# Kernel optimization log

Hardware: AMD Instinct MI355X
Metric: run time of the kernel (lower is better)

Reference implementation:

```python
import jax, jax.numpy as jnp
import numpy as np

D_MODEL = 1024
NUM_HEADS = 16
HEAD_DIM = D_MODEL // NUM_HEADS


def setup_inputs() -> dict:
    key = jax.random.key(0)
    ks = jax.random.split(key, 9)
    B, T = 2, 2048
    s = 1.0 / np.sqrt(D_MODEL)
    return {
        "x": jax.random.normal(ks[0], (B, T, D_MODEL), dtype=jnp.float32),
        "Wq": jax.random.normal(ks[1], (D_MODEL, D_MODEL), dtype=jnp.float32) * s,
        "bq": jnp.zeros((D_MODEL,), dtype=jnp.float32),
        "Wk": jax.random.normal(ks[2], (D_MODEL, D_MODEL), dtype=jnp.float32) * s,
        "bk": jnp.zeros((D_MODEL,), dtype=jnp.float32),
        "Wv": jax.random.normal(ks[3], (D_MODEL, D_MODEL), dtype=jnp.float32) * s,
        "bv": jnp.zeros((D_MODEL,), dtype=jnp.float32),
        "Wo": jax.random.normal(ks[4], (D_MODEL, D_MODEL), dtype=jnp.float32) * s,
        "bo": jnp.zeros((D_MODEL,), dtype=jnp.float32),
    }


def reference(x, Wq, bq, Wk, bk, Wv, bv, Wo, bo):
    B, T, D = x.shape
    H, Hd = NUM_HEADS, HEAD_DIM
    # Linear projections; weights stored as [in, out] (torch Linear transposed)
    q = (x @ Wq + bq).reshape(B, T, H, Hd)
    k = (x @ Wk + bk).reshape(B, T, H, Hd)
    v = (x @ Wv + bv).reshape(B, T, H, Hd)
    scale = 1.0 / jnp.sqrt(jnp.asarray(Hd, dtype=x.dtype))
    scores = jnp.einsum("bqhd,bkhd->bhqk", q, k) * scale  # [B,H,T,T]
    attn = jax.nn.softmax(scores, axis=-1)
    ctx = jnp.einsum("bhqk,bkhd->bqhd", attn, v).reshape(B, T, D)
    return ctx @ Wo + bo
```

## Files before the change

kernel.cpp:

```cpp
#include <hip/hip_runtime.h>


typedef unsigned short ushort_t;
typedef __attribute__((ext_vector_type(8))) short bf16x8;
typedef __attribute__((ext_vector_type(4))) short bf16x4;
typedef __attribute__((ext_vector_type(4))) float f32x4;

#define BATCH 2
#define SEQ   2048
#define DM    1024
#define NH    16
#define HD    64
#define MTOT  (BATCH*SEQ)

#if __has_builtin(__builtin_amdgcn_exp2f)
#define EXP2(x) __builtin_amdgcn_exp2f(x)
#else
#define EXP2(x) exp2f(x)
#endif

__device__ __forceinline__ ushort_t f2bf(float f) {
    union { float f; unsigned int u; } v; v.f = f;
    unsigned int r = v.u + 0x7fffu + ((v.u >> 16) & 1u);
    return (ushort_t)(r >> 16);
}

__device__ __forceinline__ void gload_lds16(const void* g, void* l) {
    __builtin_amdgcn_global_load_lds(
        (const __attribute__((address_space(1))) unsigned int*)g,
        (__attribute__((address_space(3))) unsigned int*)l, 16, 0, 0);
}

__global__ __launch_bounds__(256) void prep_kernel(const float* __restrict__ x,
                                                   const float* __restrict__ W0,
                                                   const float* __restrict__ W1,
                                                   const float* __restrict__ W2,
                                                   const float* __restrict__ W3,
                                                   ushort_t* __restrict__ xb,
                                                   ushort_t* __restrict__ Wtb) {
    __shared__ ushort_t tile[64][72];
    int bid = blockIdx.x, tid = threadIdx.x;
    if (bid < 4096) {
        int i = bid * 256 + tid;
        float4 v = ((const float4*)x)[i];
        ushort4 o;
        o.x = f2bf(v.x); o.y = f2bf(v.y); o.z = f2bf(v.z); o.w = f2bf(v.w);
        ((ushort4*)xb)[i] = o;
        return;
    }
    int b2 = bid - 4096;
    const float* Ws[4] = {W0, W1, W2, W3};
    const float* W = Ws[b2 >> 8];
    ushort_t* Wt = Wtb + (size_t)(b2 >> 8) * DM * DM;
    int k0 = ((b2 >> 4) & 15) * 64, n0 = (b2 & 15) * 64;
    int tr = tid >> 4;
    int tc = (tid & 15) * 4;
#pragma unroll
    for (int j = 0; j < 4; j++) {
        int r = j * 16 + tr;
        float4 v = *(const float4*)&W[(size_t)(k0 + r) * DM + n0 + tc];
        tile[r][tc + 0] = f2bf(v.x); tile[r][tc + 1] = f2bf(v.y);
        tile[r][tc + 2] = f2bf(v.z); tile[r][tc + 3] = f2bf(v.w);
    }
    __syncthreads();
#pragma unroll
    for (int j = 0; j < 4; j++) {
        int n = j * 16 + tr;
        ushort4 o;
        o.x = tile[tc + 0][n]; o.y = tile[tc + 1][n];
        o.z = tile[tc + 2][n]; o.w = tile[tc + 3][n];
        *(ushort4*)&Wt[(size_t)(n0 + n) * DM + k0 + tc] = o;
    }
}

__global__ __launch_bounds__(256) void gemm_qkv(const ushort_t* __restrict__ A,
                                                const ushort_t* __restrict__ Wtb,
                                                const float* __restrict__ bq,
                                                const float* __restrict__ bk,
                                                const float* __restrict__ bv,
                                                ushort_t* __restrict__ qo,
                                                ushort_t* __restrict__ ko,
                                                ushort_t* __restrict__ vo) {
    __shared__ ushort_t As[3][128 * 32];
    __shared__ ushort_t Bs[3][128 * 32];
    int sel = blockIdx.x >> 3;
    const ushort_t* Wt = Wtb + (size_t)sel * DM * DM;
    const float* bias = sel == 0 ? bq : (sel == 1 ? bk : bv);
    int tid = threadIdx.x;
    int w = tid >> 6, lane = tid & 63, lr = lane & 15, lg = lane >> 4;
    int wr = w >> 1, wc = w & 1;
    int m0 = blockIdx.y * 128, n0 = (blockIdx.x & 7) * 128;

    int srow = (w * 2) * 16 + (lane >> 2);
    int scb = (lane & 3) * 8;
    const ushort_t* ag = &A[(size_t)(m0 + srow) * DM + scb];
    const ushort_t* bg = &Wt[(size_t)(n0 + srow) * DM + scb];
    int ldst = (w * 2) * 1024;

    f32x4 acc[4][4] = {};

#pragma unroll
    for (int p = 0; p < 2; p++) {
        gload_lds16(ag + (size_t)p * 16 * DM, (char*)As[0] + ldst + p * 1024);
        gload_lds16(bg + (size_t)p * 16 * DM, (char*)Bs[0] + ldst + p * 1024);
    }

    int cur = 0;
    for (int kt = 0; kt < 32; ++kt) {
        if (kt + 1 < 32) {
            int nxt = cur + 1 == 3 ? 0 : cur + 1;
            int k0 = (kt + 1) << 5;
#pragma unroll
            for (int p = 0; p < 2; p++) {
                gload_lds16(ag + (size_t)p * 16 * DM + k0, (char*)As[nxt] + ldst + p * 1024);
                gload_lds16(bg + (size_t)p * 16 * DM + k0, (char*)Bs[nxt] + ldst + p * 1024);
            }
            __builtin_amdgcn_sched_barrier(0);
            asm volatile("s_waitcnt vmcnt(4)" ::: "memory");
        } else {
            __builtin_amdgcn_sched_barrier(0);
            asm volatile("s_waitcnt vmcnt(0)" ::: "memory");
        }
        __builtin_amdgcn_s_barrier();
        __builtin_amdgcn_sched_barrier(0);

        bf16x8 af[4], bfr[4];
#pragma unroll
        for (int i = 0; i < 4; i++) {
            af[i]  = *(const bf16x8*)&As[cur][(wr * 64 + i * 16 + lr) * 32 + lg * 8];
            bfr[i] = *(const bf16x8*)&Bs[cur][(wc * 64 + i * 16 + lr) * 32 + lg * 8];
        }
#pragma unroll
        for (int mi = 0; mi < 4; mi++)
#pragma unroll
            for (int ni = 0; ni < 4; ni++)
                acc[mi][ni] = __builtin_amdgcn_mfma_f32_16x16x32_bf16(
                    af[mi], bfr[ni], acc[mi][ni], 0, 0, 0);
        cur = cur + 1 == 3 ? 0 : cur + 1;
    }

    float scale = (sel == 0) ? 0.125f * 1.44269504f : 1.0f;
#pragma unroll
    for (int mi = 0; mi < 4; mi++) {
#pragma unroll
        for (int ni = 0; ni < 4; ni++) {
            f32x4 a = acc[mi][ni];
            int n = n0 + wc * 64 + ni * 16 + lr;
            float bs = bias[n];
            int mbase = m0 + wr * 64 + mi * 16 + lg * 4;
            int hh = n >> 6, d = n & 63;
            if (sel == 2) {
                int b = mbase >> 11, tt = mbase & 2047;
                size_t base = ((size_t)(b * NH + hh) * HD + d) * SEQ + tt;
                ushort4 pk;
                pk.x = f2bf(a[0] + bs); pk.y = f2bf(a[1] + bs);
                pk.z = f2bf(a[2] + bs); pk.w = f2bf(a[3] + bs);
                *(ushort4*)&vo[base] = pk;
            } else {
                ushort_t* o = sel ? ko : qo;
#pragma unroll
                for (int r = 0; r < 4; r++) {
                    int m = mbase + r;
                    int b = m >> 11, tt = m & 2047;
                    o[((size_t)(b * NH + hh) * SEQ + tt) * HD + d] =
                        f2bf((a[r] + bs) * scale);
                }
            }
        }
    }
}

__global__ __launch_bounds__(256) void gemm_out(const ushort_t* __restrict__ A,
                                                const ushort_t* __restrict__ Wt,
                                                const float* __restrict__ bias,
                                                float* __restrict__ out) {
    __shared__ ushort_t As[3][128 * 32];
    __shared__ ushort_t Bs[3][128 * 32];
    int tid = threadIdx.x;
    int w = tid >> 6, lane = tid & 63, lr = lane & 15, lg = lane >> 4;
    int wr = w >> 1, wc = w & 1;
    int m0 = blockIdx.y * 128, n0 = blockIdx.x * 128;

    int srow = (w * 2) * 16 + (lane >> 2);
    int scb = (lane & 3) * 8;
    const ushort_t* ag = &A[(size_t)(m0 + srow) * DM + scb];
    const ushort_t* bg = &Wt[(size_t)(n0 + srow) * DM + scb];
    int ldst = (w * 2) * 1024;

    f32x4 acc[4][4] = {};

#pragma unroll
    for (int p = 0; p < 2; p++) {
        gload_lds16(ag + (size_t)p * 16 * DM, (char*)As[0] + ldst + p * 1024);
        gload_lds16(bg + (size_t)p * 16 * DM, (char*)Bs[0] + ldst + p * 1024);
    }

    int cur = 0;
    for (int kt = 0; kt < 32; ++kt) {
        if (kt + 1 < 32) {
            int nxt = cur + 1 == 3 ? 0 : cur + 1;
            int k0 = (kt + 1) << 5;
#pragma unroll
            for (int p = 0; p < 2; p++) {
                gload_lds16(ag + (size_t)p * 16 * DM + k0, (char*)As[nxt] + ldst + p * 1024);
                gload_lds16(bg + (size_t)p * 16 * DM + k0, (char*)Bs[nxt] + ldst + p * 1024);
            }
            __builtin_amdgcn_sched_barrier(0);
            asm volatile("s_waitcnt vmcnt(4)" ::: "memory");
        } else {
            __builtin_amdgcn_sched_barrier(0);
            asm volatile("s_waitcnt vmcnt(0)" ::: "memory");
        }
        __builtin_amdgcn_s_barrier();
        __builtin_amdgcn_sched_barrier(0);

        bf16x8 af[4], bfr[4];
#pragma unroll
        for (int i = 0; i < 4; i++) {
            af[i]  = *(const bf16x8*)&As[cur][(wr * 64 + i * 16 + lr) * 32 + lg * 8];
            bfr[i] = *(const bf16x8*)&Bs[cur][(wc * 64 + i * 16 + lr) * 32 + lg * 8];
        }
#pragma unroll
        for (int mi = 0; mi < 4; mi++)
#pragma unroll
            for (int ni = 0; ni < 4; ni++)
                acc[mi][ni] = __builtin_amdgcn_mfma_f32_16x16x32_bf16(
                    af[mi], bfr[ni], acc[mi][ni], 0, 0, 0);
        cur = cur + 1 == 3 ? 0 : cur + 1;
    }

#pragma unroll
    for (int mi = 0; mi < 4; mi++) {
#pragma unroll
        for (int ni = 0; ni < 4; ni++) {
            f32x4 a = acc[mi][ni];
            int n = n0 + wc * 64 + ni * 16 + lr;
            float bs = bias[n];
            int mbase = m0 + wr * 64 + mi * 16 + lg * 4;
#pragma unroll
            for (int r = 0; r < 4; r++)
                out[(size_t)(mbase + r) * DM + n] = a[r] + bs;
        }
    }
}

__device__ __forceinline__ void softmax_pack(f32x4 (&s)[8], float& l_run,
                                             int4 (&pwv)[4]) {
    float rs0 = 0.f, rs1 = 0.f, rs2 = 0.f, rs3 = 0.f;
#pragma unroll
    for (int nt = 0; nt < 8; ++nt) {
        float p0 = EXP2(s[nt][0]);
        float p1 = EXP2(s[nt][1]);
        float p2 = EXP2(s[nt][2]);
        float p3 = EXP2(s[nt][3]);
        s[nt][0] = p0; s[nt][1] = p1; s[nt][2] = p2; s[nt][3] = p3;
        rs0 += p0; rs1 += p1; rs2 += p2; rs3 += p3;
    }
    float rs = (rs0 + rs1) + (rs2 + rs3);
    rs += __shfl_xor(rs, 16);
    rs += __shfl_xor(rs, 32);
    l_run += rs;
#pragma unroll
    for (int kk = 0; kk < 4; ++kk) {
        unsigned pw[4];
#pragma unroll
        for (int hh = 0; hh < 2; ++hh)
#pragma unroll
            for (int pr = 0; pr < 2; ++pr) {
                unsigned rr;
                asm("v_cvt_pk_bf16_f32 %0, %1, %2"
                    : "=v"(rr)
                    : "v"(s[kk + 4 * hh][2 * pr]), "v"(s[kk + 4 * hh][2 * pr + 1]));
                pw[hh * 2 + pr] = rr;
            }
        pwv[kk] = make_int4(pw[0], pw[1], pw[2], pw[3]);
    }
}

__global__ __launch_bounds__(512, 2) void attn_kernel(const ushort_t* __restrict__ Q,
                                                      const ushort_t* __restrict__ Kb,
                                                      const ushort_t* __restrict__ Vt,
                                                      ushort_t* __restrict__ Ctx) {
    __shared__ ushort_t Ks[2][128 * 64];
    __shared__ ushort_t Vs[2][64 * 128];

    int tid = threadIdx.x, w = tid >> 6, lane = tid & 63, lr = lane & 15, lg = lane >> 4;
    int orig = blockIdx.x;
    int wg = (orig & 7) * 32 + (orig >> 3);
    int qb = wg & 7, bh = wg >> 3;
    int q0 = qb * 256;

    const ushort_t* Qp = Q + (size_t)bh * SEQ * HD;
    const ushort_t* Kp = Kb + (size_t)bh * SEQ * HD;
    const ushort_t* Vp = Vt + (size_t)bh * HD * SEQ;

    int qrow = q0 + w * 16 + lr;
    bf16x8 aqA[2], aqB[2];
    aqA[0] = *(const bf16x8*)&Qp[(size_t)qrow * HD + lg * 8];
    aqA[1] = *(const bf16x8*)&Qp[(size_t)qrow * HD + 32 + lg * 8];
    aqB[0] = *(const bf16x8*)&Qp[(size_t)(qrow + 128) * HD + lg * 8];
    aqB[1] = *(const bf16x8*)&Qp[(size_t)(qrow + 128) * HD + 32 + lg * 8];

    f32x4 oaccA[4] = {}, oaccB[4] = {};
    float lA = 0.f, lB = 0.f;

    int krow = tid >> 3, kch = tid & 7;
    int kbyte = krow * 128 + ((kch * 16) ^ ((krow & 7) << 4));
    const ushort_t* kg0 = &Kp[(size_t)krow * HD + kch * 8];
    const ushort_t* kg1 = &Kp[(size_t)(krow + 64) * HD + kch * 8];
    int vrow = tid >> 4, vch = tid & 15;
    int S_a2 = (((vch >> 1) & 3) * 32 + (vch & 1) * 16 + (vch >> 3) * 4) * 2;
    int vswz = (vrow & 7) << 4;
    int vbyte0 = vrow * 256 + (S_a2 ^ vswz);
    int vbyte1 = vrow * 256 + ((S_a2 + 16) ^ vswz);
    const ushort_t* vg0 = &Vp[(size_t)vrow * SEQ + vch * 8];
    const ushort_t* vg1 = &Vp[(size_t)(vrow + 32) * SEQ + vch * 8];

    {
        bf16x8 k0v = *(const bf16x8*)kg0;
        bf16x8 k1v = *(const bf16x8*)kg1;
        bf16x8 v0v = *(const bf16x8*)vg0;
        bf16x8 v1v = *(const bf16x8*)vg1;
        *(bf16x8*)((char*)Ks[0] + kbyte) = k0v;
        *(bf16x8*)((char*)Ks[0] + kbyte + 64 * 128) = k1v;
        union { bf16x8 v; bf16x4 h[2]; } u0, u1;
        u0.v = v0v; u1.v = v1v;
        *(bf16x4*)((char*)Vs[0] + vbyte0) = u0.h[0];
        *(bf16x4*)((char*)Vs[0] + vbyte1) = u0.h[1];
        *(bf16x4*)((char*)Vs[0] + vbyte0 + 32 * 256) = u1.h[0];
        *(bf16x4*)((char*)Vs[0] + vbyte1 + 32 * 256) = u1.h[1];
    }
    __syncthreads();

    int kread = lr * 128;
    int kswz = (lr & 7) << 4;

    for (int t = 0; t < SEQ / 128; ++t) {
        int cur = t & 1;
        bf16x8 kr0, kr1, vr0, vr1;
        bool more = (t + 1 < SEQ / 128);
        if (more) {
            size_t ko_off = (size_t)(t + 1) * 128 * HD;
            int vo_off = (t + 1) * 128;
            kr0 = *(const bf16x8*)(kg0 + ko_off);
            kr1 = *(const bf16x8*)(kg1 + ko_off);
            vr0 = *(const bf16x8*)(vg0 + vo_off);
            vr1 = *(const bf16x8*)(vg1 + vo_off);
        }

        f32x4 sA[8], sB[8];
        __builtin_amdgcn_s_setprio(1);
#pragma unroll
        for (int nt = 0; nt < 8; ++nt) {
            f32x4 a = {}, b = {};
#pragma unroll
            for (int kk = 0; kk < 2; ++kk) {
                bf16x8 bk = *(const bf16x8*)((char*)Ks[cur] + nt * 2048 + kread +
                                             ((kk * 64 + lg * 16) ^ kswz));
                a = __builtin_amdgcn_mfma_f32_16x16x32_bf16(bk, aqA[kk], a, 0, 0, 0);
                b = __builtin_amdgcn_mfma_f32_16x16x32_bf16(bk, aqB[kk], b, 0, 0, 0);
            }
            sA[nt] = a; sB[nt] = b;
        }
        __builtin_amdgcn_s_setprio(0);

        int4 pwvA[4], pwvB[4];
        softmax_pack(sA, lA, pwvA);
        softmax_pack(sB, lB, pwvB);

        __builtin_amdgcn_s_setprio(1);
#pragma unroll
        for (int dt = 0; dt < 4; ++dt) {
            int vbase = (dt * 16 + lr) * 256;
#pragma unroll
            for (int kk = 0; kk < 4; ++kk) {
                bf16x8 bv = *(const bf16x8*)((char*)Vs[cur] + vbase +
                                             ((kk * 64 + lg * 16) ^ kswz));
                oaccA[dt] = __builtin_amdgcn_mfma_f32_16x16x32_bf16(
                    *(bf16x8*)&pwvA[kk], bv, oaccA[dt], 0, 0, 0);
                oaccB[dt] = __builtin_amdgcn_mfma_f32_16x16x32_bf16(
                    *(bf16x8*)&pwvB[kk], bv, oaccB[dt], 0, 0, 0);
            }
        }
        __builtin_amdgcn_s_setprio(0);

        if (more) {
            char* kd = (char*)Ks[cur ^ 1];
            char* vd = (char*)Vs[cur ^ 1];
            *(bf16x8*)(kd + kbyte) = kr0;
            *(bf16x8*)(kd + kbyte + 64 * 128) = kr1;
            union { bf16x8 v; bf16x4 h[2]; } u0, u1;
            u0.v = vr0; u1.v = vr1;
            *(bf16x4*)(vd + vbyte0) = u0.h[0];
            *(bf16x4*)(vd + vbyte1) = u0.h[1];
            *(bf16x4*)(vd + vbyte0 + 32 * 256) = u1.h[0];
            *(bf16x4*)(vd + vbyte1 + 32 * 256) = u1.h[1];
            __syncthreads();
        }
    }

    float invA = 1.0f / lA, invB = 1.0f / lB;
    float ivA[4], ivB[4];
#pragma unroll
    for (int r = 0; r < 4; ++r) {
        ivA[r] = __shfl(invA, lg * 4 + r);
        ivB[r] = __shfl(invB, lg * 4 + r);
    }
    int b = bh >> 4, h = bh & 15;
#pragma unroll
    for (int dt = 0; dt < 4; ++dt)
#pragma unroll
        for (int r = 0; r < 4; ++r) {
            int q = q0 + w * 16 + lg * 4 + r;
            Ctx[((size_t)(b * SEQ + q)) * DM + h * HD + dt * 16 + lr] =
                f2bf(oaccA[dt][r] * ivA[r]);
            Ctx[((size_t)(b * SEQ + q + 128)) * DM + h * HD + dt * 16 + lr] =
                f2bf(oaccB[dt][r] * ivB[r]);
        }
}

extern "C" void kernel_launch(void* const* d_in, const int* in_sizes, int n_in,
                              void* d_out, int out_size, void* d_ws, size_t ws_size,
                              hipStream_t stream) {
    const float* x  = (const float*)d_in[0];
    const float* Wq = (const float*)d_in[1];
    const float* bq = (const float*)d_in[2];
    const float* Wk = (const float*)d_in[3];
    const float* bk = (const float*)d_in[4];
    const float* Wv = (const float*)d_in[5];
    const float* bv = (const float*)d_in[6];
    const float* Wo = (const float*)d_in[7];
    const float* bo = (const float*)d_in[8];
    float* out = (float*)d_out;

    ushort_t* xbf = (ushort_t*)d_ws;
    ushort_t* wtb = xbf + (size_t)MTOT * DM;
    ushort_t* qbf = wtb + (size_t)4 * DM * DM;
    ushort_t* kbf = qbf + (size_t)MTOT * DM;
    ushort_t* vtb = kbf + (size_t)MTOT * DM;
    ushort_t* ctx = vtb + (size_t)MTOT * DM;

    prep_kernel<<<4096 + 1024, 256, 0, stream>>>(x, Wq, Wk, Wv, Wo, xbf, wtb);

    gemm_qkv<<<dim3(24, 32), 256, 0, stream>>>(xbf, wtb, bq, bk, bv, qbf, kbf, vtb);

    attn_kernel<<<256, 512, 0, stream>>>(qbf, kbf, vtb, ctx);

    gemm_out<<<dim3(8, 32), 256, 0, stream>>>(ctx, wtb + (size_t)3 * DM * DM, bo, out);
}
```

Before: 119.0 us.

## Software-pipeline attention: overlap previous tile's PV MFMAs with current QK

Restructures the attention KV loop so each iteration first computes QK^T scores for tile t, then runs the P·V MFMAs for tile t-1, and only then does softmax for tile t. The goal is to keep the matrix units busy while the exp/max softmax work runs, rather than serialising QK, softmax and PV. V gets a third LDS buffer because the previous tile's V must stay live while the next one is written. The loop is unrolled by two to ping-pong the packed P registers, with a final PV step after the loop. In exchange it uses more LDS and more registers per block, which risks spills under the 512-thread, 2-blocks-per-CU launch bound.

```diff
diff --git a/kernel.cpp b/kernel.cpp
--- a/kernel.cpp
+++ b/kernel.cpp
@@ -12,6 +12,7 @@
 #define NH    16
 #define HD    64
 #define MTOT  (BATCH*SEQ)
+#define NTILE (SEQ/128)
 
 #if __has_builtin(__builtin_amdgcn_exp2f)
 #define EXP2(x) __builtin_amdgcn_exp2f(x)
@@ -277,12 +278,88 @@
     }
 }
 
+__device__ __forceinline__ void attn_tile(
+    int t, bool first,
+    const ushort_t* kg0, const ushort_t* kg1,
+    const ushort_t* vg0, const ushort_t* vg1,
+    char* KsB, char* VsB,
+    int kbyte, int vbyte0, int vbyte1, int kread, int kswz, int lg,
+    bf16x8 (&aqA)[2], bf16x8 (&aqB)[2],
+    f32x4 (&oaccA)[4], f32x4 (&oaccB)[4], float& lA, float& lB,
+    int4 (&ppA)[4], int4 (&ppB)[4],
+    int4 (&opA)[4], int4 (&opB)[4])
+{
+    bool more = (t + 1 < NTILE);
+    bf16x8 kr0, kr1, vr0, vr1;
+    if (more) {
+        size_t ko_off = (size_t)(t + 1) * 128 * HD;
+        int vo_off = (t + 1) * 128;
+        kr0 = *(const bf16x8*)(kg0 + ko_off);
+        kr1 = *(const bf16x8*)(kg1 + ko_off);
+        vr0 = *(const bf16x8*)(vg0 + vo_off);
+        vr1 = *(const bf16x8*)(vg1 + vo_off);
+    }
+
+    char* KsCur = KsB + (t & 1) * 16384;
+    f32x4 sA[8], sB[8];
+    __builtin_amdgcn_s_setprio(1);
+#pragma unroll
+    for (int nt = 0; nt < 8; ++nt) {
+        f32x4 a = {}, b = {};
+#pragma unroll
+        for (int kk = 0; kk < 2; ++kk) {
+            bf16x8 bk = *(const bf16x8*)(KsCur + nt * 2048 + kread +
+                                         ((kk * 64 + lg * 16) ^ kswz));
+            a = __builtin_amdgcn_mfma_f32_16x16x32_bf16(bk, aqA[kk], a, 0, 0, 0);
+            b = __builtin_amdgcn_mfma_f32_16x16x32_bf16(bk, aqB[kk], b, 0, 0, 0);
+        }
+        sA[nt] = a; sB[nt] = b;
+    }
+    __builtin_amdgcn_s_setprio(0);
+
+    if (!first) {
+        char* VsPrev = VsB + ((t + 2) % 3) * 16384;
+        __builtin_amdgcn_s_setprio(1);
+#pragma unroll
+        for (int dt = 0; dt < 4; ++dt) {
+            int vbase = (dt * 16 + (kread >> 7)) * 256;
+#pragma unroll
+            for (int kk = 0; kk < 4; ++kk) {
+                bf16x8 bv = *(const bf16x8*)(VsPrev + vbase +
+                                             ((kk * 64 + lg * 16) ^ kswz));
+                oaccA[dt] = __builtin_amdgcn_mfma_f32_16x16x32_bf16(
+                    *(bf16x8*)&ppA[kk], bv, oaccA[dt], 0, 0, 0);
+                oaccB[dt] = __builtin_amdgcn_mfma_f32_16x16x32_bf16(
+                    *(bf16x8*)&ppB[kk], bv, oaccB[dt], 0, 0, 0);
+            }
+        }
+        __builtin_amdgcn_s_setprio(0);
+    }
+
+    softmax_pack(sA, lA, opA);
+    softmax_pack(sB, lB, opB);
+
+    if (more) {
+        char* kd = KsB + ((t + 1) & 1) * 16384;
+        char* vd = VsB + ((t + 1) % 3) * 16384;
+        *(bf16x8*)(kd + kbyte) = kr0;
+        *(bf16x8*)(kd + kbyte + 64 * 128) = kr1;
+        union { bf16x8 v; bf16x4 h[2]; } u0, u1;
+        u0.v = vr0; u1.v = vr1;
+        *(bf16x4*)(vd + vbyte0) = u0.h[0];
+        *(bf16x4*)(vd + vbyte1) = u0.h[1];
+        *(bf16x4*)(vd + vbyte0 + 32 * 256) = u1.h[0];
+        *(bf16x4*)(vd + vbyte1 + 32 * 256) = u1.h[1];
+        __syncthreads();
+    }
+}
+
 __global__ __launch_bounds__(512, 2) void attn_kernel(const ushort_t* __restrict__ Q,
                                                       const ushort_t* __restrict__ Kb,
                                                       const ushort_t* __restrict__ Vt,
                                                       ushort_t* __restrict__ Ctx) {
     __shared__ ushort_t Ks[2][128 * 64];
-    __shared__ ushort_t Vs[2][64 * 128];
+    __shared__ ushort_t Vs[3][64 * 128];
 
     int tid = threadIdx.x, w = tid >> 6, lane = tid & 63, lr = lane & 15, lg = lane >> 4;
     int orig = blockIdx.x;
@@ -334,68 +411,40 @@
 
     int kread = lr * 128;
     int kswz = (lr & 7) << 4;
-
-    for (int t = 0; t < SEQ / 128; ++t) {
-        int cur = t & 1;
-        bf16x8 kr0, kr1, vr0, vr1;
-        bool more = (t + 1 < SEQ / 128);
-        if (more) {
-            size_t ko_off = (size_t)(t + 1) * 128 * HD;
-            int vo_off = (t + 1) * 128;
-            kr0 = *(const bf16x8*)(kg0 + ko_off);
-            kr1 = *(const bf16x8*)(kg1 + ko_off);
-            vr0 = *(const bf16x8*)(vg0 + vo_off);
-            vr1 = *(const bf16x8*)(vg1 + vo_off);
-        }
-
-        f32x4 sA[8], sB[8];
-        __builtin_amdgcn_s_setprio(1);
-#pragma unroll
-        for (int nt = 0; nt < 8; ++nt) {
-            f32x4 a = {}, b = {};
-#pragma unroll
-            for (int kk = 0; kk < 2; ++kk) {
-                bf16x8 bk = *(const bf16x8*)((char*)Ks[cur] + nt * 2048 + kread +
-                                             ((kk * 64 + lg * 16) ^ kswz));
-                a = __builtin_amdgcn_mfma_f32_16x16x32_bf16(bk, aqA[kk], a, 0, 0, 0);
-                b = __builtin_amdgcn_mfma_f32_16x16x32_bf16(bk, aqB[kk], b, 0, 0, 0);
-            }
-            sA[nt] = a; sB[nt] = b;
-        }
-        __builtin_amdgcn_s_setprio(0);
-
-        int4 pwvA[4], pwvB[4];
-        softmax_pack(sA, lA, pwvA);
-        softmax_pack(sB, lB, pwvB);
-
-        __builtin_amdgcn_s_setprio(1);
+    char* KsB = (char*)Ks[0];
+    char* VsB = (char*)Vs[0];
+
+    int4 pA0[4], pB0[4], pA1[4], pB1[4];
+
+    attn_tile(0, true, kg0, kg1, vg0, vg1, KsB, VsB, kbyte, vbyte0, vbyte1,
+              kread, kswz, lg, aqA, aqB, oaccA, oaccB, lA, lB,
+              pA1, pB1, pA0, pB0);
+    for (int t = 1; t < NTILE - 1; t += 2) {
+        attn_tile(t, false, kg0, kg1, vg0, vg1, KsB, VsB, kbyte, vbyte0, vbyte1,
+                  kread, kswz, lg, aqA, aqB, oaccA, oaccB, lA, lB,
+                  pA0, pB0, pA1, pB1);
+        attn_tile(t + 1, false, kg0, kg1, vg0, vg1, KsB, VsB, kbyte, vbyte0, vbyte1,
+                  kread, kswz, lg, aqA, aqB, oaccA, oaccB, lA, lB,
+                  pA1, pB1, pA0, pB0);
+    }
+    attn_tile(NTILE - 1, false, kg0, kg1, vg0, vg1, KsB, VsB, kbyte, vbyte0, vbyte1,
+              kread, kswz, lg, aqA, aqB, oaccA, oaccB, lA, lB,
+              pA0, pB0, pA1, pB1);
+
+    {
+        char* VsLast = VsB + ((NTILE - 1) % 3) * 16384;
 #pragma unroll
         for (int dt = 0; dt < 4; ++dt) {
             int vbase = (dt * 16 + lr) * 256;
 #pragma unroll
             for (int kk = 0; kk < 4; ++kk) {
-                bf16x8 bv = *(const bf16x8*)((char*)Vs[cur] + vbase +
+                bf16x8 bv = *(const bf16x8*)(VsLast + vbase +
                                              ((kk * 64 + lg * 16) ^ kswz));
                 oaccA[dt] = __builtin_amdgcn_mfma_f32_16x16x32_bf16(
-                    *(bf16x8*)&pwvA[kk], bv, oaccA[dt], 0, 0, 0);
+                    *(bf16x8*)&pA1[kk], bv, oaccA[dt], 0, 0, 0);
                 oaccB[dt] = __builtin_amdgcn_mfma_f32_16x16x32_bf16(
-                    *(bf16x8*)&pwvB[kk], bv, oaccB[dt], 0, 0, 0);
-            }
-        }
-        __builtin_amdgcn_s_setprio(0);
-
-        if (more) {
-            char* kd = (char*)Ks[cur ^ 1];
-            char* vd = (char*)Vs[cur ^ 1];
-            *(bf16x8*)(kd + kbyte) = kr0;
-            *(bf16x8*)(kd + kbyte + 64 * 128) = kr1;
-            union { bf16x8 v; bf16x4 h[2]; } u0, u1;
-            u0.v = vr0; u1.v = vr1;
-            *(bf16x4*)(vd + vbyte0) = u0.h[0];
-            *(bf16x4*)(vd + vbyte1) = u0.h[1];
-            *(bf16x4*)(vd + vbyte0 + 32 * 256) = u1.h[0];
-            *(bf16x4*)(vd + vbyte1 + 32 * 256) = u1.h[1];
-            __syncthreads();
+                    *(bf16x8*)&pB1[kk], bv, oaccB[dt], 0, 0, 0);
+            }
         }
     }
 
```

Result: no change. 119.4 us (+0.3%).

## Switch attention kernel to 32x32x16 MFMA tiles with reworked V LDS layout

Applied to the files above, without the earlier changes.

Rewrites the attention inner loop to use 32x32x16 bf16 MFMA instructions instead of pairs of 16x16x32. Each wave now owns 32 contiguous query rows, and the K/V LDS read patterns and the V write swizzle are changed to match the new operand layout. The softmax row-sum needs only one cross-lane shuffle instead of two. The larger MFMA tile reduces instruction count and LDS operand reads per FLOP, but it changes register usage and risks layout bugs in the new index math.

```diff
diff --git a/kernel.cpp b/kernel.cpp
--- a/kernel.cpp
+++ b/kernel.cpp
@@ -5,6 +5,7 @@
 typedef __attribute__((ext_vector_type(8))) short bf16x8;
 typedef __attribute__((ext_vector_type(4))) short bf16x4;
 typedef __attribute__((ext_vector_type(4))) float f32x4;
+typedef __attribute__((ext_vector_type(16))) float f32x16;
 
 #define BATCH 2
 #define SEQ   2048
@@ -12,6 +13,7 @@
 #define NH    16
 #define HD    64
 #define MTOT  (BATCH*SEQ)
+#define NTILE (SEQ/128)
 
 #if __has_builtin(__builtin_amdgcn_exp2f)
 #define EXP2(x) __builtin_amdgcn_exp2f(x)
@@ -244,39 +246,6 @@
     }
 }
 
-__device__ __forceinline__ void softmax_pack(f32x4 (&s)[8], float& l_run,
-                                             int4 (&pwv)[4]) {
-    float rs0 = 0.f, rs1 = 0.f, rs2 = 0.f, rs3 = 0.f;
-#pragma unroll
-    for (int nt = 0; nt < 8; ++nt) {
-        float p0 = EXP2(s[nt][0]);
-        float p1 = EXP2(s[nt][1]);
-        float p2 = EXP2(s[nt][2]);
-        float p3 = EXP2(s[nt][3]);
-        s[nt][0] = p0; s[nt][1] = p1; s[nt][2] = p2; s[nt][3] = p3;
-        rs0 += p0; rs1 += p1; rs2 += p2; rs3 += p3;
-    }
-    float rs = (rs0 + rs1) + (rs2 + rs3);
-    rs += __shfl_xor(rs, 16);
-    rs += __shfl_xor(rs, 32);
-    l_run += rs;
-#pragma unroll
-    for (int kk = 0; kk < 4; ++kk) {
-        unsigned pw[4];
-#pragma unroll
-        for (int hh = 0; hh < 2; ++hh)
-#pragma unroll
-            for (int pr = 0; pr < 2; ++pr) {
-                unsigned rr;
-                asm("v_cvt_pk_bf16_f32 %0, %1, %2"
-                    : "=v"(rr)
-                    : "v"(s[kk + 4 * hh][2 * pr]), "v"(s[kk + 4 * hh][2 * pr + 1]));
-                pw[hh * 2 + pr] = rr;
-            }
-        pwv[kk] = make_int4(pw[0], pw[1], pw[2], pw[3]);
-    }
-}
-
 __global__ __launch_bounds__(512, 2) void attn_kernel(const ushort_t* __restrict__ Q,
                                                       const ushort_t* __restrict__ Kb,
                                                       const ushort_t* __restrict__ Vt,
@@ -284,7 +253,9 @@
     __shared__ ushort_t Ks[2][128 * 64];
     __shared__ ushort_t Vs[2][64 * 128];
 
-    int tid = threadIdx.x, w = tid >> 6, lane = tid & 63, lr = lane & 15, lg = lane >> 4;
+    int tid = threadIdx.x, w = tid >> 6, lane = tid & 63;
+    int lq = lane & 31;
+    int kh = lane >> 5;
     int orig = blockIdx.x;
     int wg = (orig & 7) * 32 + (orig >> 3);
     int qb = wg & 7, bh = wg >> 3;
@@ -294,25 +265,24 @@
     const ushort_t* Kp = Kb + (size_t)bh * SEQ * HD;
     const ushort_t* Vp = Vt + (size_t)bh * HD * SEQ;
 
-    int qrow = q0 + w * 16 + lr;
-    bf16x8 aqA[2], aqB[2];
-    aqA[0] = *(const bf16x8*)&Qp[(size_t)qrow * HD + lg * 8];
-    aqA[1] = *(const bf16x8*)&Qp[(size_t)qrow * HD + 32 + lg * 8];
-    aqB[0] = *(const bf16x8*)&Qp[(size_t)(qrow + 128) * HD + lg * 8];
-    aqB[1] = *(const bf16x8*)&Qp[(size_t)(qrow + 128) * HD + 32 + lg * 8];
-
-    f32x4 oaccA[4] = {}, oaccB[4] = {};
-    float lA = 0.f, lB = 0.f;
+    int qrow = q0 + w * 32 + lq;
+    bf16x8 aq[4];
+#pragma unroll
+    for (int c = 0; c < 4; ++c)
+        aq[c] = *(const bf16x8*)&Qp[(size_t)qrow * HD + c * 16 + kh * 8];
+
+    f32x16 oacc0 = {}, oacc1 = {};
+    float l_run = 0.f;
 
     int krow = tid >> 3, kch = tid & 7;
     int kbyte = krow * 128 + ((kch * 16) ^ ((krow & 7) << 4));
     const ushort_t* kg0 = &Kp[(size_t)krow * HD + kch * 8];
     const ushort_t* kg1 = &Kp[(size_t)(krow + 64) * HD + kch * 8];
     int vrow = tid >> 4, vch = tid & 15;
-    int S_a2 = (((vch >> 1) & 3) * 32 + (vch & 1) * 16 + (vch >> 3) * 4) * 2;
+    int B0 = 64 * (vch >> 2) + 32 * ((vch >> 1) & 1) + 8 * (vch & 1);
     int vswz = (vrow & 7) << 4;
-    int vbyte0 = vrow * 256 + (S_a2 ^ vswz);
-    int vbyte1 = vrow * 256 + ((S_a2 + 16) ^ vswz);
+    int vbyte0 = vrow * 256 + (B0 ^ vswz);
+    int vbyte1 = vrow * 256 + ((B0 + 16) ^ vswz);
     const ushort_t* vg0 = &Vp[(size_t)vrow * SEQ + vch * 8];
     const ushort_t* vg1 = &Vp[(size_t)(vrow + 32) * SEQ + vch * 8];
 
@@ -332,13 +302,12 @@
     }
     __syncthreads();
 
-    int kread = lr * 128;
-    int kswz = (lr & 7) << 4;
-
-    for (int t = 0; t < SEQ / 128; ++t) {
+    int lsw = (lq & 7) << 4;
+
+    for (int t = 0; t < NTILE; ++t) {
         int cur = t & 1;
         bf16x8 kr0, kr1, vr0, vr1;
-        bool more = (t + 1 < SEQ / 128);
+        bool more = (t + 1 < NTILE);
         if (more) {
             size_t ko_off = (size_t)(t + 1) * 128 * HD;
             int vo_off = (t + 1) * 128;
@@ -348,39 +317,62 @@
             vr1 = *(const bf16x8*)(vg1 + vo_off);
         }
 
-        f32x4 sA[8], sB[8];
+        f32x16 s[4];
         __builtin_amdgcn_s_setprio(1);
 #pragma unroll
-        for (int nt = 0; nt < 8; ++nt) {
-            f32x4 a = {}, b = {};
-#pragma unroll
-            for (int kk = 0; kk < 2; ++kk) {
-                bf16x8 bk = *(const bf16x8*)((char*)Ks[cur] + nt * 2048 + kread +
-                                             ((kk * 64 + lg * 16) ^ kswz));
-                a = __builtin_amdgcn_mfma_f32_16x16x32_bf16(bk, aqA[kk], a, 0, 0, 0);
-                b = __builtin_amdgcn_mfma_f32_16x16x32_bf16(bk, aqB[kk], b, 0, 0, 0);
-            }
-            sA[nt] = a; sB[nt] = b;
+        for (int tau = 0; tau < 4; ++tau) {
+            f32x16 a = {};
+            int kb = (tau * 32 + lq) * 128;
+#pragma unroll
+            for (int c = 0; c < 4; ++c) {
+                bf16x8 ak = *(const bf16x8*)((char*)Ks[cur] + kb +
+                                             ((c * 32 + kh * 16) ^ lsw));
+                a = __builtin_amdgcn_mfma_f32_32x32x16_bf16(ak, aq[c], a, 0, 0, 0);
+            }
+            s[tau] = a;
         }
         __builtin_amdgcn_s_setprio(0);
 
-        int4 pwvA[4], pwvB[4];
-        softmax_pack(sA, lA, pwvA);
-        softmax_pack(sB, lB, pwvB);
+        int4 pp[8];
+        float rsum = 0.f;
+#pragma unroll
+        for (int tau = 0; tau < 4; ++tau) {
+            float pe[16];
+            float r0 = 0.f, r1 = 0.f, r2 = 0.f, r3 = 0.f;
+#pragma unroll
+            for (int e = 0; e < 16; e += 4) {
+                pe[e + 0] = EXP2(s[tau][e + 0]);
+                pe[e + 1] = EXP2(s[tau][e + 1]);
+                pe[e + 2] = EXP2(s[tau][e + 2]);
+                pe[e + 3] = EXP2(s[tau][e + 3]);
+                r0 += pe[e + 0]; r1 += pe[e + 1];
+                r2 += pe[e + 2]; r3 += pe[e + 3];
+            }
+            rsum += (r0 + r1) + (r2 + r3);
+            unsigned pw0[4], pw1[4];
+#pragma unroll
+            for (int wd = 0; wd < 4; ++wd) {
+                asm("v_cvt_pk_bf16_f32 %0, %1, %2"
+                    : "=v"(pw0[wd]) : "v"(pe[2 * wd]), "v"(pe[2 * wd + 1]));
+                asm("v_cvt_pk_bf16_f32 %0, %1, %2"
+                    : "=v"(pw1[wd]) : "v"(pe[8 + 2 * wd]), "v"(pe[8 + 2 * wd + 1]));
+            }
+            pp[2 * tau]     = make_int4(pw0[0], pw0[1], pw0[2], pw0[3]);
+            pp[2 * tau + 1] = make_int4(pw1[0], pw1[1], pw1[2], pw1[3]);
+        }
+        rsum += __shfl_xor(rsum, 32);
+        l_run += rsum;
 
         __builtin_amdgcn_s_setprio(1);
 #pragma unroll
-        for (int dt = 0; dt < 4; ++dt) {
-            int vbase = (dt * 16 + lr) * 256;
-#pragma unroll
-            for (int kk = 0; kk < 4; ++kk) {
-                bf16x8 bv = *(const bf16x8*)((char*)Vs[cur] + vbase +
-                                             ((kk * 64 + lg * 16) ^ kswz));
-                oaccA[dt] = __builtin_amdgcn_mfma_f32_16x16x32_bf16(
-                    *(bf16x8*)&pwvA[kk], bv, oaccA[dt], 0, 0, 0);
-                oaccB[dt] = __builtin_amdgcn_mfma_f32_16x16x32_bf16(
-                    *(bf16x8*)&pwvB[kk], bv, oaccB[dt], 0, 0, 0);
-            }
+        for (int c = 0; c < 8; ++c) {
+            int vb0 = lq * 256 + ((c * 32 + kh * 16) ^ lsw);
+            bf16x8 bv0 = *(const bf16x8*)((char*)Vs[cur] + vb0);
+            bf16x8 bv1 = *(const bf16x8*)((char*)Vs[cur] + vb0 + 32 * 256);
+            oacc0 = __builtin_amdgcn_mfma_f32_32x32x16_bf16(
+                *(bf16x8*)&pp[c], bv0, oacc0, 0, 0, 0);
+            oacc1 = __builtin_amdgcn_mfma_f32_32x32x16_bf16(
+                *(bf16x8*)&pp[c], bv1, oacc1, 0, 0, 0);
         }
         __builtin_amdgcn_s_setprio(0);
 
@@ -399,24 +391,17 @@
         }
     }
 
-    float invA = 1.0f / lA, invB = 1.0f / lB;
-    float ivA[4], ivB[4];
-#pragma unroll
-    for (int r = 0; r < 4; ++r) {
-        ivA[r] = __shfl(invA, lg * 4 + r);
-        ivB[r] = __shfl(invB, lg * 4 + r);
-    }
-    int b = bh >> 4, h = bh & 15;
-#pragma unroll
-    for (int dt = 0; dt < 4; ++dt)
-#pragma unroll
-        for (int r = 0; r < 4; ++r) {
-            int q = q0 + w * 16 + lg * 4 + r;
-            Ctx[((size_t)(b * SEQ + q)) * DM + h * HD + dt * 16 + lr] =
-                f2bf(oaccA[dt][r] * ivA[r]);
-            Ctx[((size_t)(b * SEQ + q + 128)) * DM + h * HD + dt * 16 + lr] =
-                f2bf(oaccB[dt][r] * ivB[r]);
-        }
+    float inv = 1.0f / l_run;
+    int b = bh >> 4, hd_ = bh & 15;
+#pragma unroll
+    for (int r = 0; r < 16; ++r) {
+        int qloc = (r & 3) + 8 * (r >> 2) + 4 * kh;
+        float iv = __shfl(inv, qloc);
+        int q = q0 + w * 32 + qloc;
+        size_t base = ((size_t)(b * SEQ + q)) * DM + hd_ * HD + lq;
+        Ctx[base]      = f2bf(oacc0[r] * iv);
+        Ctx[base + 32] = f2bf(oacc1[r] * iv);
+    }
 }
 
 extern "C" void kernel_launch(void* const* d_in, const int* in_sizes, int n_in,
```

Result: no change. 121.2 us (+1.8%).

## Drop LDS staging in attention; read K and pre-tiled V directly from global

Applied to the files above, without the earlier changes.

The QKV projection now writes V in a per-128-key tiled layout with the permutation the PV MFMA operand expects, so the attention kernel can load V fragments straight from global memory. The attention kernel drops the shared-memory double buffer and barriers and reads K and V fragments directly from global (L2/cache) inside the loop. It also splits the QK/softmax into separate A and B passes to cut live registers. This removes LDS writes and syncs but relies on cache for the reuse that LDS gave across the eight waves, which risks more global traffic and exposed load latency.

```diff
diff --git a/kernel.cpp b/kernel.cpp
--- a/kernel.cpp
+++ b/kernel.cpp
@@ -3,7 +3,6 @@
 
 typedef unsigned short ushort_t;
 typedef __attribute__((ext_vector_type(8))) short bf16x8;
-typedef __attribute__((ext_vector_type(4))) short bf16x4;
 typedef __attribute__((ext_vector_type(4))) float f32x4;
 
 #define BATCH 2
@@ -12,6 +11,7 @@
 #define NH    16
 #define HD    64
 #define MTOT  (BATCH*SEQ)
+#define NTILE (SEQ/128)
 
 #if __has_builtin(__builtin_amdgcn_exp2f)
 #define EXP2(x) __builtin_amdgcn_exp2f(x)
@@ -151,7 +151,11 @@
             int hh = n >> 6, d = n & 63;
             if (sel == 2) {
                 int b = mbase >> 11, tt = mbase & 2047;
-                size_t base = ((size_t)(b * NH + hh) * HD + d) * SEQ + tt;
+                int kap = tt & 127;
+                int slot = 32 * ((kap >> 4) & 3) + 8 * ((kap >> 2) & 3) + 4 * (kap >> 6);
+                size_t base = (size_t)(b * NH + hh) * SEQ * HD
+                            + (size_t)(tt >> 7) * (128 * HD)
+                            + (size_t)d * 128 + slot;
                 ushort4 pk;
                 pk.x = f2bf(a[0] + bs); pk.y = f2bf(a[1] + bs);
                 pk.z = f2bf(a[2] + bs); pk.w = f2bf(a[3] + bs);
@@ -281,9 +285,6 @@
                                                       const ushort_t* __restrict__ Kb,
                                                       const ushort_t* __restrict__ Vt,
                                                       ushort_t* __restrict__ Ctx) {
-    __shared__ ushort_t Ks[2][128 * 64];
-    __shared__ ushort_t Vs[2][64 * 128];
-
     int tid = threadIdx.x, w = tid >> 6, lane = tid & 63, lr = lane & 15, lg = lane >> 4;
     int orig = blockIdx.x;
     int wg = (orig & 7) * 32 + (orig >> 3);
@@ -292,7 +293,7 @@
 
     const ushort_t* Qp = Q + (size_t)bh * SEQ * HD;
     const ushort_t* Kp = Kb + (size_t)bh * SEQ * HD;
-    const ushort_t* Vp = Vt + (size_t)bh * HD * SEQ;
+    const ushort_t* Vp = Vt + (size_t)bh * SEQ * HD;
 
     int qrow = q0 + w * 16 + lr;
     bf16x8 aqA[2], aqB[2];
@@ -304,99 +305,58 @@
     f32x4 oaccA[4] = {}, oaccB[4] = {};
     float lA = 0.f, lB = 0.f;
 
-    int krow = tid >> 3, kch = tid & 7;
-    int kbyte = krow * 128 + ((kch * 16) ^ ((krow & 7) << 4));
-    const ushort_t* kg0 = &Kp[(size_t)krow * HD + kch * 8];
-    const ushort_t* kg1 = &Kp[(size_t)(krow + 64) * HD + kch * 8];
-    int vrow = tid >> 4, vch = tid & 15;
-    int S_a2 = (((vch >> 1) & 3) * 32 + (vch & 1) * 16 + (vch >> 3) * 4) * 2;
-    int vswz = (vrow & 7) << 4;
-    int vbyte0 = vrow * 256 + (S_a2 ^ vswz);
-    int vbyte1 = vrow * 256 + ((S_a2 + 16) ^ vswz);
-    const ushort_t* vg0 = &Vp[(size_t)vrow * SEQ + vch * 8];
-    const ushort_t* vg1 = &Vp[(size_t)(vrow + 32) * SEQ + vch * 8];
-
-    {
-        bf16x8 k0v = *(const bf16x8*)kg0;
-        bf16x8 k1v = *(const bf16x8*)kg1;
-        bf16x8 v0v = *(const bf16x8*)vg0;
-        bf16x8 v1v = *(const bf16x8*)vg1;
-        *(bf16x8*)((char*)Ks[0] + kbyte) = k0v;
-        *(bf16x8*)((char*)Ks[0] + kbyte + 64 * 128) = k1v;
-        union { bf16x8 v; bf16x4 h[2]; } u0, u1;
-        u0.v = v0v; u1.v = v1v;
-        *(bf16x4*)((char*)Vs[0] + vbyte0) = u0.h[0];
-        *(bf16x4*)((char*)Vs[0] + vbyte1) = u0.h[1];
-        *(bf16x4*)((char*)Vs[0] + vbyte0 + 32 * 256) = u1.h[0];
-        *(bf16x4*)((char*)Vs[0] + vbyte1 + 32 * 256) = u1.h[1];
-    }
-    __syncthreads();
-
-    int kread = lr * 128;
-    int kswz = (lr & 7) << 4;
-
-    for (int t = 0; t < SEQ / 128; ++t) {
-        int cur = t & 1;
-        bf16x8 kr0, kr1, vr0, vr1;
-        bool more = (t + 1 < SEQ / 128);
-        if (more) {
-            size_t ko_off = (size_t)(t + 1) * 128 * HD;
-            int vo_off = (t + 1) * 128;
-            kr0 = *(const bf16x8*)(kg0 + ko_off);
-            kr1 = *(const bf16x8*)(kg1 + ko_off);
-            vr0 = *(const bf16x8*)(vg0 + vo_off);
-            vr1 = *(const bf16x8*)(vg1 + vo_off);
-        }
-
-        f32x4 sA[8], sB[8];
+    for (int t = 0; t < NTILE; ++t) {
+        const ushort_t* Kt = Kp + (size_t)t * 128 * HD;
+        const ushort_t* Vtl = Vp + (size_t)t * 128 * HD;
+
+        f32x4 sA[8];
         __builtin_amdgcn_s_setprio(1);
 #pragma unroll
         for (int nt = 0; nt < 8; ++nt) {
-            f32x4 a = {}, b = {};
+            f32x4 a = {};
 #pragma unroll
             for (int kk = 0; kk < 2; ++kk) {
-                bf16x8 bk = *(const bf16x8*)((char*)Ks[cur] + nt * 2048 + kread +
-                                             ((kk * 64 + lg * 16) ^ kswz));
+                bf16x8 bk = *(const bf16x8*)&Kt[(size_t)(nt * 16 + lr) * HD +
+                                                kk * 32 + lg * 8];
                 a = __builtin_amdgcn_mfma_f32_16x16x32_bf16(bk, aqA[kk], a, 0, 0, 0);
+            }
+            sA[nt] = a;
+        }
+        __builtin_amdgcn_s_setprio(0);
+        int4 ppA[4];
+        softmax_pack(sA, lA, ppA);
+
+        f32x4 sB[8];
+        __builtin_amdgcn_s_setprio(1);
+#pragma unroll
+        for (int nt = 0; nt < 8; ++nt) {
+            f32x4 b = {};
+#pragma unroll
+            for (int kk = 0; kk < 2; ++kk) {
+                bf16x8 bk = *(const bf16x8*)&Kt[(size_t)(nt * 16 + lr) * HD +
+                                                kk * 32 + lg * 8];
                 b = __builtin_amdgcn_mfma_f32_16x16x32_bf16(bk, aqB[kk], b, 0, 0, 0);
             }
-            sA[nt] = a; sB[nt] = b;
+            sB[nt] = b;
         }
         __builtin_amdgcn_s_setprio(0);
-
-        int4 pwvA[4], pwvB[4];
-        softmax_pack(sA, lA, pwvA);
-        softmax_pack(sB, lB, pwvB);
+        int4 ppB[4];
+        softmax_pack(sB, lB, ppB);
 
         __builtin_amdgcn_s_setprio(1);
 #pragma unroll
         for (int dt = 0; dt < 4; ++dt) {
-            int vbase = (dt * 16 + lr) * 256;
+            const ushort_t* vr = Vtl + (size_t)(dt * 16 + lr) * 128;
 #pragma unroll
             for (int kk = 0; kk < 4; ++kk) {
-                bf16x8 bv = *(const bf16x8*)((char*)Vs[cur] + vbase +
-                                             ((kk * 64 + lg * 16) ^ kswz));
+                bf16x8 bv = *(const bf16x8*)&vr[kk * 32 + lg * 8];
                 oaccA[dt] = __builtin_amdgcn_mfma_f32_16x16x32_bf16(
-                    *(bf16x8*)&pwvA[kk], bv, oaccA[dt], 0, 0, 0);
+                    *(bf16x8*)&ppA[kk], bv, oaccA[dt], 0, 0, 0);
                 oaccB[dt] = __builtin_amdgcn_mfma_f32_16x16x32_bf16(
-                    *(bf16x8*)&pwvB[kk], bv, oaccB[dt], 0, 0, 0);
+                    *(bf16x8*)&ppB[kk], bv, oaccB[dt], 0, 0, 0);
             }
         }
         __builtin_amdgcn_s_setprio(0);
-
-        if (more) {
-            char* kd = (char*)Ks[cur ^ 1];
-            char* vd = (char*)Vs[cur ^ 1];
-            *(bf16x8*)(kd + kbyte) = kr0;
-            *(bf16x8*)(kd + kbyte + 64 * 128) = kr1;
-            union { bf16x8 v; bf16x4 h[2]; } u0, u1;
-            u0.v = vr0; u1.v = vr1;
-            *(bf16x4*)(vd + vbyte0) = u0.h[0];
-            *(bf16x4*)(vd + vbyte1) = u0.h[1];
-            *(bf16x4*)(vd + vbyte0 + 32 * 256) = u1.h[0];
-            *(bf16x4*)(vd + vbyte1 + 32 * 256) = u1.h[1];
-            __syncthreads();
-        }
     }
 
     float invA = 1.0f / lA, invB = 1.0f / lB;
```

After: 250.1 us. 2.1x slower.
